# Optimization experiments

Hardware: AMD Instinct MI355X
Metric: run time of the kernel (lower is better)

The kernel has to match this reference:

```python
import jax, jax.numpy as jnp
import numpy as np

B, C, I, E = 2048, 256, 9, 10


def _contraction(U_list, W_list, x, y):
    """Recursive symmetric contraction for one output irrep.
    U_list/W_list ordered [U1, U2, U3] (correlation 1..3).
    x: [b, c, i], y: [b, e]. Returns flattened [b, c * m].
    """
    U3, W3 = U_list[-1], W_list[-1]
    # main: '...ik,ekc,bci,be->bc...'
    out = jnp.einsum('...ik,ekc,bci,be->bc...', U3, W3, x, y)
    for corr in range(len(U_list) - 2, -1, -1):
        U, W = U_list[corr], W_list[corr]
        # weighting: '...k,ekc,be->bc...'
        c_tensor = jnp.einsum('...k,ekc,be->bc...', U, W, y) + out
        # contract: 'bc...i,bci->bc...'
        out = jnp.einsum('bc...i,bci->bc...', c_tensor, x)
    return out.reshape(out.shape[0], -1)


def setup_inputs() -> dict:
    key = jax.random.key(0)
    ks = jax.random.split(key, 14)
    inp = {
        'x': jax.random.normal(ks[0], (B, C, I), jnp.float32),
        'y': jax.random.uniform(ks[1], (B, E), jnp.float32),
        'U1_s': jax.random.normal(ks[2], (I, 1), jnp.float32),
        'U2_s': jax.random.normal(ks[3], (I, I, 3), jnp.float32),
        'U3_s': jax.random.normal(ks[4], (I, I, I, 23), jnp.float32),
        'U1_v': jax.random.normal(ks[5], (3, I, 1), jnp.float32),
        'U2_v': jax.random.normal(ks[6], (3, I, I, 4), jnp.float32),
        'U3_v': jax.random.normal(ks[7], (3, I, I, I, 30), jnp.float32),
        'W1_s': jax.random.normal(ks[8], (E, 1, C), jnp.float32),
        'W2_s': jax.random.normal(ks[9], (E, 3, C), jnp.float32) / 3.0,
        'W3_s': jax.random.normal(ks[10], (E, 23, C), jnp.float32) / 23.0,
        'W1_v': jax.random.normal(ks[11], (E, 1, C), jnp.float32),
        'W2_v': jax.random.normal(ks[12], (E, 4, C), jnp.float32) / 4.0,
        'W3_v': jax.random.normal(ks[13], (E, 30, C), jnp.float32) / 30.0,
    }
    return inp


def reference(x, y, U1_s, U2_s, U3_s, U1_v, U2_v, U3_v,
              W1_s, W2_s, W3_s, W1_v, W2_v, W3_v):
    out_s = _contraction([U1_s, U2_s, U3_s], [W1_s, W2_s, W3_s], x, y)  # [b, c]
    out_v = _contraction([U1_v, U2_v, U3_v], [W1_v, W2_v, W3_v], x, y)  # [b, c*3]
    return jnp.concatenate([out_s, out_v], axis=-1)  # [b, 4c]
```

## Files before the change

kernel.cpp:

```cpp
#include <hip/hip_runtime.h>
#include <hip/hip_bf16.h>


#define NB 2048
#define NC 256
#define NI 9
#define NE 10

#define N_TRI 165
#define N_PAIR 45

#define T3N (N_TRI * NE * NC)
#define T2N (N_PAIR * NE * NC)
#define T1N (NI * NE * NC)

__global__ __launch_bounds__(256) void sc_prep(
    const float* __restrict__ U1_s, const float* __restrict__ U2_s,
    const float* __restrict__ U3_s, const float* __restrict__ U1_v,
    const float* __restrict__ U2_v, const float* __restrict__ U3_v,
    const float* __restrict__ W1_s, const float* __restrict__ W2_s,
    const float* __restrict__ W3_s, const float* __restrict__ W1_v,
    const float* __restrict__ W2_v, const float* __restrict__ W3_v,
    float* __restrict__ ws)
{
    const int m = blockIdx.x;
    const int e = blockIdx.y;
    const int tid = threadIdx.x;
    float4* __restrict__ T3 = (float4*)ws;
    float4* __restrict__ T2 = T3 + T3N;
    float4* __restrict__ T1 = T2 + T2N;

    __shared__ float sym[128];

    if (m < N_TRI) {
        if (tid < 113) {
            int ii = 0, jj = 0, kk = 0, cnt = 0;
            for (int i = 0; i < NI; i++)
                for (int j = i; j < NI; j++)
                    for (int k = j; k < NI; k++) {
                        if (cnt == m) { ii = i; jj = j; kk = k; }
                        cnt++;
                    }
            int P[6][3]; int np;
            if (ii == jj && jj == kk) {
                np = 1;
                P[0][0] = ii; P[0][1] = ii; P[0][2] = ii;
            } else if (ii == jj) {
                np = 3;
                P[0][0] = ii; P[0][1] = ii; P[0][2] = kk;
                P[1][0] = ii; P[1][1] = kk; P[1][2] = ii;
                P[2][0] = kk; P[2][1] = ii; P[2][2] = ii;
            } else if (jj == kk) {
                np = 3;
                P[0][0] = ii; P[0][1] = jj; P[0][2] = jj;
                P[1][0] = jj; P[1][1] = ii; P[1][2] = jj;
                P[2][0] = jj; P[2][1] = jj; P[2][2] = ii;
            } else {
                np = 6;
                P[0][0] = ii; P[0][1] = jj; P[0][2] = kk;
                P[1][0] = ii; P[1][1] = kk; P[1][2] = jj;
                P[2][0] = jj; P[2][1] = ii; P[2][2] = kk;
                P[3][0] = jj; P[3][1] = kk; P[3][2] = ii;
                P[4][0] = kk; P[4][1] = ii; P[4][2] = jj;
                P[5][0] = kk; P[5][1] = jj; P[5][2] = ii;
            }
            float s = 0.f;
            if (tid < 23) {
                for (int p = 0; p < np; p++)
                    s += U3_s[((P[p][0] * NI + P[p][1]) * NI + P[p][2]) * 23 + tid];
            } else {
                int a = (tid - 23) / 30, t = (tid - 23) % 30;
                for (int p = 0; p < np; p++)
                    s += U3_v[(((a * NI + P[p][0]) * NI + P[p][1]) * NI + P[p][2]) * 30 + t];
            }
            sym[tid] = s;
        }
        __syncthreads();
        const int c = tid;
        float s = 0.f, v0 = 0.f, v1 = 0.f, v2 = 0.f;
        #pragma unroll
        for (int t = 0; t < 23; t++)
            s = fmaf(sym[t], W3_s[(e * 23 + t) * NC + c], s);
        #pragma unroll
        for (int t = 0; t < 30; t++) {
            float wv = W3_v[(e * 30 + t) * NC + c];
            v0 = fmaf(sym[23 + t],      wv, v0);
            v1 = fmaf(sym[53 + t],      wv, v1);
            v2 = fmaf(sym[83 + t],      wv, v2);
        }
        T3[(m * NE + e) * NC + c] = make_float4(s, v0, v1, v2);
    } else if (m < N_TRI + N_PAIR) {
        const int mm = m - N_TRI;
        if (tid < 15) {
            int ii = 0, jj = 0, cnt = 0;
            for (int i = 0; i < NI; i++)
                for (int j = i; j < NI; j++) {
                    if (cnt == mm) { ii = i; jj = j; }
                    cnt++;
                }
            float s;
            if (tid < 3) {
                s = U2_s[(ii * NI + jj) * 3 + tid];
                if (ii != jj) s += U2_s[(jj * NI + ii) * 3 + tid];
            } else {
                int a = (tid - 3) / 4, t = (tid - 3) % 4;
                s = U2_v[((a * NI + ii) * NI + jj) * 4 + t];
                if (ii != jj) s += U2_v[((a * NI + jj) * NI + ii) * 4 + t];
            }
            sym[tid] = s;
        }
        __syncthreads();
        const int c = tid;
        float s = 0.f, v0 = 0.f, v1 = 0.f, v2 = 0.f;
        #pragma unroll
        for (int t = 0; t < 3; t++)
            s = fmaf(sym[t], W2_s[(e * 3 + t) * NC + c], s);
        #pragma unroll
        for (int t = 0; t < 4; t++) {
            float wv = W2_v[(e * 4 + t) * NC + c];
            v0 = fmaf(sym[3 + t],  wv, v0);
            v1 = fmaf(sym[7 + t],  wv, v1);
            v2 = fmaf(sym[11 + t], wv, v2);
        }
        T2[(mm * NE + e) * NC + c] = make_float4(s, v0, v1, v2);
    } else {
        const int i = m - N_TRI - N_PAIR;
        const int c = tid;
        float w1s = W1_s[e * NC + c], w1v = W1_v[e * NC + c];
        T1[(i * NE + e) * NC + c] = make_float4(
            U1_s[i] * w1s,
            U1_v[0 * NI + i] * w1v,
            U1_v[1 * NI + i] * w1v,
            U1_v[2 * NI + i] * w1v);
    }
}

#define BT 8
__global__ __launch_bounds__(128) void sc_main(
    const float* __restrict__ x, const float* __restrict__ y,
    const float* __restrict__ ws, float* __restrict__ out)
{
    const int tid = threadIdx.x;
    const int tx  = tid & 63;
    const int tyu = __builtin_amdgcn_readfirstlane(tid >> 6);
    const int bid = blockIdx.x;
    const int xcd    = bid & 7;
    const int c_tile = xcd >> 1;
    const int b_tile = ((bid >> 3) << 1) | (xcd & 1);
    const int c  = (c_tile << 6) + tx;
    const int b0 = (b_tile << 4) + (tyu << 3);

    __shared__ float xs[2][NI][BT][64];
    #pragma unroll
    for (int n = 0; n < BT; n++) {
        const float* xp = x + ((size_t)(b0 + n) * NC + c) * NI;
        #pragma unroll
        for (int i = 0; i < NI; i++) xs[tyu][i][n][tx] = xp[i];
    }

    float w[NE][BT];
    #pragma unroll
    for (int n = 0; n < BT; n++)
        #pragma unroll
        for (int e = 0; e < NE; e++) w[e][n] = y[(b0 + n) * NE + e];

    float acc[BT][4];
    #pragma unroll
    for (int n = 0; n < BT; n++)
        #pragma unroll
        for (int h = 0; h < 4; h++) acc[n][h] = 0.f;

    const float4* __restrict__ T3 = (const float4*)ws;
    const float4* __restrict__ T2 = T3 + T3N;
    const float4* __restrict__ T1 = T2 + T2N;

    {
        float4 tc[NE];
        #pragma unroll
        for (int e = 0; e < NE; e++) tc[e] = T3[e * NC + c];
        int i = 0, j = 0, k = 0;
        for (int m = 0; m < N_TRI; m++) {
            const int mn = (m == N_TRI - 1) ? m : m + 1;
            float4 tn[NE];
            #pragma unroll
            for (int e = 0; e < NE; e++) tn[e] = T3[(mn * NE + e) * NC + c];
            float phi[BT];
            #pragma unroll
            for (int n = 0; n < BT; n++)
                phi[n] = xs[tyu][i][n][tx] * xs[tyu][j][n][tx] * xs[tyu][k][n][tx];
            #pragma unroll
            for (int e = 0; e < NE; e++) {
                const float4 t = tc[e];
                #pragma unroll
                for (int n = 0; n < BT; n++) {
                    const float p = w[e][n] * phi[n];
                    acc[n][0] = fmaf(p, t.x, acc[n][0]);
                    acc[n][1] = fmaf(p, t.y, acc[n][1]);
                    acc[n][2] = fmaf(p, t.z, acc[n][2]);
                    acc[n][3] = fmaf(p, t.w, acc[n][3]);
                }
            }
            #pragma unroll
            for (int e = 0; e < NE; e++) tc[e] = tn[e];
            k++;
            if (k == NI) { j++; if (j == NI) { i++; j = i; } k = j; }
        }
    }

    {
        float4 tc[NE];
        #pragma unroll
        for (int e = 0; e < NE; e++) tc[e] = T2[e * NC + c];
        int i = 0, j = 0;
        for (int m = 0; m < N_PAIR; m++) {
            const int mn = (m == N_PAIR - 1) ? m : m + 1;
            float4 tn[NE];
            #pragma unroll
            for (int e = 0; e < NE; e++) tn[e] = T2[(mn * NE + e) * NC + c];
            float phi[BT];
            #pragma unroll
            for (int n = 0; n < BT; n++)
                phi[n] = xs[tyu][i][n][tx] * xs[tyu][j][n][tx];
            #pragma unroll
            for (int e = 0; e < NE; e++) {
                const float4 t = tc[e];
                #pragma unroll
                for (int n = 0; n < BT; n++) {
                    const float p = w[e][n] * phi[n];
                    acc[n][0] = fmaf(p, t.x, acc[n][0]);
                    acc[n][1] = fmaf(p, t.y, acc[n][1]);
                    acc[n][2] = fmaf(p, t.z, acc[n][2]);
                    acc[n][3] = fmaf(p, t.w, acc[n][3]);
                }
            }
            #pragma unroll
            for (int e = 0; e < NE; e++) tc[e] = tn[e];
            j++;
            if (j == NI) { i++; j = i; }
        }
    }

    for (int i = 0; i < NI; i++) {
        float4 tc[NE];
        #pragma unroll
        for (int e = 0; e < NE; e++) tc[e] = T1[(i * NE + e) * NC + c];
        float phi[BT];
        #pragma unroll
        for (int n = 0; n < BT; n++) phi[n] = xs[tyu][i][n][tx];
        #pragma unroll
        for (int e = 0; e < NE; e++) {
            const float4 t = tc[e];
            #pragma unroll
            for (int n = 0; n < BT; n++) {
                const float p = w[e][n] * phi[n];
                acc[n][0] = fmaf(p, t.x, acc[n][0]);
                acc[n][1] = fmaf(p, t.y, acc[n][1]);
                acc[n][2] = fmaf(p, t.z, acc[n][2]);
                acc[n][3] = fmaf(p, t.w, acc[n][3]);
            }
        }
    }

    #pragma unroll
    for (int n = 0; n < BT; n++) {
        float* ob = out + (size_t)(b0 + n) * (4 * NC);
        ob[c] = acc[n][0];
        ob[NC + 3 * c + 0] = acc[n][1];
        ob[NC + 3 * c + 1] = acc[n][2];
        ob[NC + 3 * c + 2] = acc[n][3];
    }
}

extern "C" void kernel_launch(void* const* d_in, const int* in_sizes, int n_in,
                              void* d_out, int out_size, void* d_ws, size_t ws_size,
                              hipStream_t stream) {
    const float* x    = (const float*)d_in[0];
    const float* y    = (const float*)d_in[1];
    const float* U1_s = (const float*)d_in[2];
    const float* U2_s = (const float*)d_in[3];
    const float* U3_s = (const float*)d_in[4];
    const float* U1_v = (const float*)d_in[5];
    const float* U2_v = (const float*)d_in[6];
    const float* U3_v = (const float*)d_in[7];
    const float* W1_s = (const float*)d_in[8];
    const float* W2_s = (const float*)d_in[9];
    const float* W3_s = (const float*)d_in[10];
    const float* W1_v = (const float*)d_in[11];
    const float* W2_v = (const float*)d_in[12];
    const float* W3_v = (const float*)d_in[13];
    float* out = (float*)d_out;
    float* ws  = (float*)d_ws;

    sc_prep<<<dim3(N_TRI + N_PAIR + NI, NE), 256, 0, stream>>>(
        U1_s, U2_s, U3_s, U1_v, U2_v, U3_v,
        W1_s, W2_s, W3_s, W1_v, W2_v, W3_v, ws);
    sc_main<<<NB / 16 * (NC / 64), 128, 0, stream>>>(x, y, ws, out);
}
```

Baseline: 305.7 us.

## Split outputs into two grid halves and reassociate e-sum with packed FMA

The precomputed T tables are split into two float2 halves, each covering two of the four output channels, and a second grid dimension launches one half per block, doubling the block count. The inner loop is reassociated: it first sums T[e]*y[e] over e with packed v2f FMAs and then multiplies once by phi, instead of forming w*phi for every e and doing four scalar FMAs. The m-loop is unrolled by two with explicit double buffers. The cost is recomputing phi and reloading x and y in both halves, and writing non-contiguous output pieces per half.

```diff
diff --git a/kernel.cpp b/kernel.cpp
--- a/kernel.cpp
+++ b/kernel.cpp
@@ -9,10 +9,16 @@
 
 #define N_TRI 165
 #define N_PAIR 45
-
-#define T3N (N_TRI * NE * NC)
-#define T2N (N_PAIR * NE * NC)
-#define T1N (NI * NE * NC)
+#define BT 8
+
+typedef float v2f __attribute__((ext_vector_type(2)));
+
+#define A3N (N_TRI * NE * NC)
+#define A2N (N_PAIR * NE * NC)
+#define A1N (NI * NE * NC)
+#define PARTN (A3N + A2N + A1N)
+
+__device__ __forceinline__ v2f splat2(float s) { v2f r; r.x = s; r.y = s; return r; }
 
 __global__ __launch_bounds__(256) void sc_prep(
     const float* __restrict__ U1_s, const float* __restrict__ U2_s,
@@ -26,9 +32,9 @@
     const int m = blockIdx.x;
     const int e = blockIdx.y;
     const int tid = threadIdx.x;
-    float4* __restrict__ T3 = (float4*)ws;
-    float4* __restrict__ T2 = T3 + T3N;
-    float4* __restrict__ T1 = T2 + T2N;
+    float2* __restrict__ TA3 = (float2*)ws;
+    float2* __restrict__ TA2 = TA3 + A3N;
+    float2* __restrict__ TA1 = TA2 + A2N;
 
     __shared__ float sym[128];
 
@@ -84,11 +90,12 @@
         #pragma unroll
         for (int t = 0; t < 30; t++) {
             float wv = W3_v[(e * 30 + t) * NC + c];
-            v0 = fmaf(sym[23 + t],      wv, v0);
-            v1 = fmaf(sym[53 + t],      wv, v1);
-            v2 = fmaf(sym[83 + t],      wv, v2);
-        }
-        T3[(m * NE + e) * NC + c] = make_float4(s, v0, v1, v2);
+            v0 = fmaf(sym[23 + t], wv, v0);
+            v1 = fmaf(sym[53 + t], wv, v1);
+            v2 = fmaf(sym[83 + t], wv, v2);
+        }
+        TA3[(m * NE + e) * NC + c] = make_float2(s, v0);
+        TA3[(m * NE + e) * NC + c + PARTN] = make_float2(v1, v2);
     } else if (m < N_TRI + N_PAIR) {
         const int mm = m - N_TRI;
         if (tid < 15) {
@@ -122,20 +129,30 @@
             v1 = fmaf(sym[7 + t],  wv, v1);
             v2 = fmaf(sym[11 + t], wv, v2);
         }
-        T2[(mm * NE + e) * NC + c] = make_float4(s, v0, v1, v2);
+        TA2[(mm * NE + e) * NC + c] = make_float2(s, v0);
+        TA2[(mm * NE + e) * NC + c + PARTN] = make_float2(v1, v2);
     } else {
         const int i = m - N_TRI - N_PAIR;
         const int c = tid;
         float w1s = W1_s[e * NC + c], w1v = W1_v[e * NC + c];
-        T1[(i * NE + e) * NC + c] = make_float4(
-            U1_s[i] * w1s,
-            U1_v[0 * NI + i] * w1v,
-            U1_v[1 * NI + i] * w1v,
-            U1_v[2 * NI + i] * w1v);
+        TA1[(i * NE + e) * NC + c] = make_float2(U1_s[i] * w1s,
+                                                 U1_v[0 * NI + i] * w1v);
+        TA1[(i * NE + e) * NC + c + PARTN] = make_float2(U1_v[1 * NI + i] * w1v,
+                                                         U1_v[2 * NI + i] * w1v);
     }
 }
 
-#define BT 8
+__device__ __forceinline__ void step_acc(const v2f (&buf)[NE], float phi,
+                                         const float* __restrict__ wn,
+                                         v2f& acc)
+{
+    v2f ts = buf[0] * splat2(wn[0]);
+    #pragma unroll
+    for (int e = 1; e < NE; e++)
+        ts = __builtin_elementwise_fma(buf[e], splat2(wn[e]), ts);
+    acc = __builtin_elementwise_fma(splat2(phi), ts, acc);
+}
+
 __global__ __launch_bounds__(128) void sc_main(
     const float* __restrict__ x, const float* __restrict__ y,
     const float* __restrict__ ws, float* __restrict__ out)
@@ -143,10 +160,11 @@
     const int tid = threadIdx.x;
     const int tx  = tid & 63;
     const int tyu = __builtin_amdgcn_readfirstlane(tid >> 6);
-    const int bid = blockIdx.x;
-    const int xcd    = bid & 7;
+    const int bx  = blockIdx.x;
+    const int part = blockIdx.y;
+    const int xcd    = bx & 7;
     const int c_tile = xcd >> 1;
-    const int b_tile = ((bid >> 3) << 1) | (xcd & 1);
+    const int b_tile = ((bx >> 3) << 1) | (xcd & 1);
     const int c  = (c_tile << 6) + tx;
     const int b0 = (b_tile << 4) + (tyu << 3);
 
@@ -157,117 +175,111 @@
         #pragma unroll
         for (int i = 0; i < NI; i++) xs[tyu][i][n][tx] = xp[i];
     }
-
-    float w[NE][BT];
+    const float* xb = &xs[tyu][0][0][tx];
+
+    float w[BT][NE];
     #pragma unroll
     for (int n = 0; n < BT; n++)
         #pragma unroll
-        for (int e = 0; e < NE; e++) w[e][n] = y[(b0 + n) * NE + e];
-
-    float acc[BT][4];
-    #pragma unroll
-    for (int n = 0; n < BT; n++)
-        #pragma unroll
-        for (int h = 0; h < 4; h++) acc[n][h] = 0.f;
-
-    const float4* __restrict__ T3 = (const float4*)ws;
-    const float4* __restrict__ T2 = T3 + T3N;
-    const float4* __restrict__ T1 = T2 + T2N;
+        for (int e = 0; e < NE; e++) w[n][e] = y[(b0 + n) * NE + e];
+
+    v2f acc[BT];
+    #pragma unroll
+    for (int n = 0; n < BT; n++) acc[n] = splat2(0.f);
+
+    const v2f* __restrict__ T3 = (const v2f*)ws + (size_t)part * PARTN;
+    const v2f* __restrict__ T2 = T3 + A3N;
+    const v2f* __restrict__ T1 = T2 + A2N;
 
     {
-        float4 tc[NE];
-        #pragma unroll
-        for (int e = 0; e < NE; e++) tc[e] = T3[e * NC + c];
+        v2f bufA[NE], bufB[NE];
+        #pragma unroll
+        for (int e = 0; e < NE; e++) bufA[e] = T3[e * NC + c];
         int i = 0, j = 0, k = 0;
-        for (int m = 0; m < N_TRI; m++) {
-            const int mn = (m == N_TRI - 1) ? m : m + 1;
-            float4 tn[NE];
-            #pragma unroll
-            for (int e = 0; e < NE; e++) tn[e] = T3[(mn * NE + e) * NC + c];
-            float phi[BT];
-            #pragma unroll
-            for (int n = 0; n < BT; n++)
-                phi[n] = xs[tyu][i][n][tx] * xs[tyu][j][n][tx] * xs[tyu][k][n][tx];
-            #pragma unroll
-            for (int e = 0; e < NE; e++) {
-                const float4 t = tc[e];
+        for (int m = 0; m < N_TRI - 1; m += 2) {
+            #pragma unroll
+            for (int e = 0; e < NE; e++) bufB[e] = T3[((m + 1) * NE + e) * NC + c];
+            {
+                float b1 = 0;  (void)b1;
                 #pragma unroll
                 for (int n = 0; n < BT; n++) {
-                    const float p = w[e][n] * phi[n];
-                    acc[n][0] = fmaf(p, t.x, acc[n][0]);
-                    acc[n][1] = fmaf(p, t.y, acc[n][1]);
-                    acc[n][2] = fmaf(p, t.z, acc[n][2]);
-                    acc[n][3] = fmaf(p, t.w, acc[n][3]);
+                    float ph = xb[(i * BT + n) * 64] * xb[(j * BT + n) * 64]
+                             * xb[(k * BT + n) * 64];
+                    step_acc(bufA, ph, w[n], acc[n]);
                 }
             }
-            #pragma unroll
-            for (int e = 0; e < NE; e++) tc[e] = tn[e];
-            k++;
-            if (k == NI) { j++; if (j == NI) { i++; j = i; } k = j; }
-        }
-    }
-
-    {
-        float4 tc[NE];
-        #pragma unroll
-        for (int e = 0; e < NE; e++) tc[e] = T2[e * NC + c];
-        int i = 0, j = 0;
-        for (int m = 0; m < N_PAIR; m++) {
-            const int mn = (m == N_PAIR - 1) ? m : m + 1;
-            float4 tn[NE];
-            #pragma unroll
-            for (int e = 0; e < NE; e++) tn[e] = T2[(mn * NE + e) * NC + c];
-            float phi[BT];
-            #pragma unroll
-            for (int n = 0; n < BT; n++)
-                phi[n] = xs[tyu][i][n][tx] * xs[tyu][j][n][tx];
-            #pragma unroll
-            for (int e = 0; e < NE; e++) {
-                const float4 t = tc[e];
+            k++; if (k == NI) { j++; if (j == NI) { i++; j = i; } k = j; }
+            const int mp = (m + 2 < N_TRI) ? m + 2 : N_TRI - 1;
+            #pragma unroll
+            for (int e = 0; e < NE; e++) bufA[e] = T3[(mp * NE + e) * NC + c];
+            {
                 #pragma unroll
                 for (int n = 0; n < BT; n++) {
-                    const float p = w[e][n] * phi[n];
-                    acc[n][0] = fmaf(p, t.x, acc[n][0]);
-                    acc[n][1] = fmaf(p, t.y, acc[n][1]);
-                    acc[n][2] = fmaf(p, t.z, acc[n][2]);
-                    acc[n][3] = fmaf(p, t.w, acc[n][3]);
+                    float ph = xb[(i * BT + n) * 64] * xb[(j * BT + n) * 64]
+                             * xb[(k * BT + n) * 64];
+                    step_acc(bufB, ph, w[n], acc[n]);
                 }
             }
-            #pragma unroll
-            for (int e = 0; e < NE; e++) tc[e] = tn[e];
-            j++;
-            if (j == NI) { i++; j = i; }
+            k++; if (k == NI) { j++; if (j == NI) { i++; j = i; } k = j; }
+        }
+        #pragma unroll
+        for (int n = 0; n < BT; n++) {
+            float ph = xb[(i * BT + n) * 64] * xb[(j * BT + n) * 64]
+                     * xb[(k * BT + n) * 64];
+            step_acc(bufA, ph, w[n], acc[n]);
+        }
+    }
+
+    {
+        v2f bufA[NE], bufB[NE];
+        #pragma unroll
+        for (int e = 0; e < NE; e++) bufA[e] = T2[e * NC + c];
+        int i = 0, j = 0;
+        for (int m = 0; m < N_PAIR - 1; m += 2) {
+            #pragma unroll
+            for (int e = 0; e < NE; e++) bufB[e] = T2[((m + 1) * NE + e) * NC + c];
+            #pragma unroll
+            for (int n = 0; n < BT; n++) {
+                float ph = xb[(i * BT + n) * 64] * xb[(j * BT + n) * 64];
+                step_acc(bufA, ph, w[n], acc[n]);
+            }
+            j++; if (j == NI) { i++; j = i; }
+            const int mp = (m + 2 < N_PAIR) ? m + 2 : N_PAIR - 1;
+            #pragma unroll
+            for (int e = 0; e < NE; e++) bufA[e] = T2[(mp * NE + e) * NC + c];
+            #pragma unroll
+            for (int n = 0; n < BT; n++) {
+                float ph = xb[(i * BT + n) * 64] * xb[(j * BT + n) * 64];
+                step_acc(bufB, ph, w[n], acc[n]);
+            }
+            j++; if (j == NI) { i++; j = i; }
+        }
+        #pragma unroll
+        for (int n = 0; n < BT; n++) {
+            float ph = xb[(i * BT + n) * 64] * xb[(j * BT + n) * 64];
+            step_acc(bufA, ph, w[n], acc[n]);
         }
     }
 
     for (int i = 0; i < NI; i++) {
-        float4 tc[NE];
-        #pragma unroll
-        for (int e = 0; e < NE; e++) tc[e] = T1[(i * NE + e) * NC + c];
-        float phi[BT];
-        #pragma unroll
-        for (int n = 0; n < BT; n++) phi[n] = xs[tyu][i][n][tx];
-        #pragma unroll
-        for (int e = 0; e < NE; e++) {
-            const float4 t = tc[e];
-            #pragma unroll
-            for (int n = 0; n < BT; n++) {
-                const float p = w[e][n] * phi[n];
-                acc[n][0] = fmaf(p, t.x, acc[n][0]);
-                acc[n][1] = fmaf(p, t.y, acc[n][1]);
-                acc[n][2] = fmaf(p, t.z, acc[n][2]);
-                acc[n][3] = fmaf(p, t.w, acc[n][3]);
-            }
-        }
+        v2f buf[NE];
+        #pragma unroll
+        for (int e = 0; e < NE; e++) buf[e] = T1[(i * NE + e) * NC + c];
+        #pragma unroll
+        for (int n = 0; n < BT; n++)
+            step_acc(buf, xb[(i * BT + n) * 64], w[n], acc[n]);
     }
 
     #pragma unroll
     for (int n = 0; n < BT; n++) {
         float* ob = out + (size_t)(b0 + n) * (4 * NC);
-        ob[c] = acc[n][0];
-        ob[NC + 3 * c + 0] = acc[n][1];
-        ob[NC + 3 * c + 1] = acc[n][2];
-        ob[NC + 3 * c + 2] = acc[n][3];
+        if (part == 0) {
+            ob[c] = acc[n].x;
+            ob[NC + 3 * c + 0] = acc[n].y;
+        } else {
+            ob[NC + 3 * c + 1] = acc[n].x;
+            ob[NC + 3 * c + 2] = acc[n].y;
+        }
     }
 }
 
@@ -294,5 +306,5 @@
     sc_prep<<<dim3(N_TRI + N_PAIR + NI, NE), 256, 0, stream>>>(
         U1_s, U2_s, U3_s, U1_v, U2_v, U3_v,
         W1_s, W2_s, W3_s, W1_v, W2_v, W3_v, ws);
-    sc_main<<<NB / 16 * (NC / 64), 128, 0, stream>>>(x, y, ws, out);
+    sc_main<<<dim3(512, 2), 128, 0, stream>>>(x, y, ws, out);
 }
```

Measured after the change: 480.0 us. 1.57x slower.

## Split contraction across two blocks per tile with atomic accumulation and double-buffered loads

Applied to the files above, without the earlier changes.

The main kernel now launches two blocks per (b, c) tile. One block handles the first 110 triples. The other handles the remaining triples plus the pair and single terms. Partial sums are combined with atomicAdd into an output that is zeroed by a memset first. This doubles the number of waves available to hide the latency of the precomputed-table loads. The triple and pair loops are rewritten as explicit ping-pong double buffers. The prep kernel now loops over e inside each block, so the symmetrised U is computed once per m instead of once per e. The cost is serialised prep work on fewer blocks, extra atomic traffic, and a memset launch.

```diff
diff --git a/kernel.cpp b/kernel.cpp
--- a/kernel.cpp
+++ b/kernel.cpp
@@ -9,10 +9,13 @@
 
 #define N_TRI 165
 #define N_PAIR 45
+#define BT 8
 
 #define T3N (N_TRI * NE * NC)
 #define T2N (N_PAIR * NE * NC)
 #define T1N (NI * NE * NC)
+
+#define MSPLIT 110
 
 __global__ __launch_bounds__(256) void sc_prep(
     const float* __restrict__ U1_s, const float* __restrict__ U2_s,
@@ -24,7 +27,6 @@
     float* __restrict__ ws)
 {
     const int m = blockIdx.x;
-    const int e = blockIdx.y;
     const int tid = threadIdx.x;
     float4* __restrict__ T3 = (float4*)ws;
     float4* __restrict__ T2 = T3 + T3N;
@@ -77,18 +79,20 @@
         }
         __syncthreads();
         const int c = tid;
-        float s = 0.f, v0 = 0.f, v1 = 0.f, v2 = 0.f;
-        #pragma unroll
-        for (int t = 0; t < 23; t++)
-            s = fmaf(sym[t], W3_s[(e * 23 + t) * NC + c], s);
-        #pragma unroll
-        for (int t = 0; t < 30; t++) {
-            float wv = W3_v[(e * 30 + t) * NC + c];
-            v0 = fmaf(sym[23 + t],      wv, v0);
-            v1 = fmaf(sym[53 + t],      wv, v1);
-            v2 = fmaf(sym[83 + t],      wv, v2);
-        }
-        T3[(m * NE + e) * NC + c] = make_float4(s, v0, v1, v2);
+        for (int e = 0; e < NE; e++) {
+            float s = 0.f, v0 = 0.f, v1 = 0.f, v2 = 0.f;
+            #pragma unroll
+            for (int t = 0; t < 23; t++)
+                s = fmaf(sym[t], W3_s[(e * 23 + t) * NC + c], s);
+            #pragma unroll
+            for (int t = 0; t < 30; t++) {
+                float wv = W3_v[(e * 30 + t) * NC + c];
+                v0 = fmaf(sym[23 + t], wv, v0);
+                v1 = fmaf(sym[53 + t], wv, v1);
+                v2 = fmaf(sym[83 + t], wv, v2);
+            }
+            T3[(m * NE + e) * NC + c] = make_float4(s, v0, v1, v2);
+        }
     } else if (m < N_TRI + N_PAIR) {
         const int mm = m - N_TRI;
         if (tid < 15) {
@@ -111,31 +115,116 @@
         }
         __syncthreads();
         const int c = tid;
-        float s = 0.f, v0 = 0.f, v1 = 0.f, v2 = 0.f;
-        #pragma unroll
-        for (int t = 0; t < 3; t++)
-            s = fmaf(sym[t], W2_s[(e * 3 + t) * NC + c], s);
-        #pragma unroll
-        for (int t = 0; t < 4; t++) {
-            float wv = W2_v[(e * 4 + t) * NC + c];
-            v0 = fmaf(sym[3 + t],  wv, v0);
-            v1 = fmaf(sym[7 + t],  wv, v1);
-            v2 = fmaf(sym[11 + t], wv, v2);
-        }
-        T2[(mm * NE + e) * NC + c] = make_float4(s, v0, v1, v2);
+        for (int e = 0; e < NE; e++) {
+            float s = 0.f, v0 = 0.f, v1 = 0.f, v2 = 0.f;
+            #pragma unroll
+            for (int t = 0; t < 3; t++)
+                s = fmaf(sym[t], W2_s[(e * 3 + t) * NC + c], s);
+            #pragma unroll
+            for (int t = 0; t < 4; t++) {
+                float wv = W2_v[(e * 4 + t) * NC + c];
+                v0 = fmaf(sym[3 + t],  wv, v0);
+                v1 = fmaf(sym[7 + t],  wv, v1);
+                v2 = fmaf(sym[11 + t], wv, v2);
+            }
+            T2[(mm * NE + e) * NC + c] = make_float4(s, v0, v1, v2);
+        }
     } else {
         const int i = m - N_TRI - N_PAIR;
         const int c = tid;
-        float w1s = W1_s[e * NC + c], w1v = W1_v[e * NC + c];
-        T1[(i * NE + e) * NC + c] = make_float4(
-            U1_s[i] * w1s,
-            U1_v[0 * NI + i] * w1v,
-            U1_v[1 * NI + i] * w1v,
-            U1_v[2 * NI + i] * w1v);
+        for (int e = 0; e < NE; e++) {
+            float w1s = W1_s[e * NC + c], w1v = W1_v[e * NC + c];
+            T1[(i * NE + e) * NC + c] = make_float4(
+                U1_s[i] * w1s,
+                U1_v[0 * NI + i] * w1v,
+                U1_v[1 * NI + i] * w1v,
+                U1_v[2 * NI + i] * w1v);
+        }
     }
 }
 
-#define BT 8
+__device__ __forceinline__ void tri_advance(int& i, int& j, int& k) {
+    k++;
+    if (k == NI) { j++; if (j == NI) { i++; j = i; } k = j; }
+}
+
+template <int M0, int M1, int I0, int J0, int K0>
+__device__ __forceinline__ void do_triples(
+    const float4* __restrict__ T3, int c, const float* __restrict__ xb,
+    const float (&w)[NE][BT], float (&acc)[BT][4])
+{
+    float4 bufA[NE], bufB[NE];
+    #pragma unroll
+    for (int e = 0; e < NE; e++) bufA[e] = T3[(M0 * NE + e) * NC + c];
+    int i = I0, j = J0, k = K0;
+    for (int m = M0; m + 1 < M1; m += 2) {
+        #pragma unroll
+        for (int e = 0; e < NE; e++) bufB[e] = T3[((m + 1) * NE + e) * NC + c];
+        {
+            float phi[BT];
+            #pragma unroll
+            for (int n = 0; n < BT; n++)
+                phi[n] = xb[(i * BT + n) * 64] * xb[(j * BT + n) * 64]
+                       * xb[(k * BT + n) * 64];
+            #pragma unroll
+            for (int e = 0; e < NE; e++) {
+                const float4 t = bufA[e];
+                #pragma unroll
+                for (int n = 0; n < BT; n++) {
+                    const float p = w[e][n] * phi[n];
+                    acc[n][0] = fmaf(p, t.x, acc[n][0]);
+                    acc[n][1] = fmaf(p, t.y, acc[n][1]);
+                    acc[n][2] = fmaf(p, t.z, acc[n][2]);
+                    acc[n][3] = fmaf(p, t.w, acc[n][3]);
+                }
+            }
+        }
+        tri_advance(i, j, k);
+        const int mp = (m + 2 < M1) ? m + 2 : M1 - 1;
+        #pragma unroll
+        for (int e = 0; e < NE; e++) bufA[e] = T3[(mp * NE + e) * NC + c];
+        {
+            float phi[BT];
+            #pragma unroll
+            for (int n = 0; n < BT; n++)
+                phi[n] = xb[(i * BT + n) * 64] * xb[(j * BT + n) * 64]
+                       * xb[(k * BT + n) * 64];
+            #pragma unroll
+            for (int e = 0; e < NE; e++) {
+                const float4 t = bufB[e];
+                #pragma unroll
+                for (int n = 0; n < BT; n++) {
+                    const float p = w[e][n] * phi[n];
+                    acc[n][0] = fmaf(p, t.x, acc[n][0]);
+                    acc[n][1] = fmaf(p, t.y, acc[n][1]);
+                    acc[n][2] = fmaf(p, t.z, acc[n][2]);
+                    acc[n][3] = fmaf(p, t.w, acc[n][3]);
+                }
+            }
+        }
+        tri_advance(i, j, k);
+    }
+    if ((M1 - M0) & 1) {
+        float phi[BT];
+        #pragma unroll
+        for (int n = 0; n < BT; n++)
+            phi[n] = xb[(i * BT + n) * 64] * xb[(j * BT + n) * 64]
+                   * xb[(k * BT + n) * 64];
+        #pragma unroll
+        for (int e = 0; e < NE; e++) {
+            const float4 t = bufA[e];
+            #pragma unroll
+            for (int n = 0; n < BT; n++) {
+                const float p = w[e][n] * phi[n];
+                acc[n][0] = fmaf(p, t.x, acc[n][0]);
+                acc[n][1] = fmaf(p, t.y, acc[n][1]);
+                acc[n][2] = fmaf(p, t.z, acc[n][2]);
+                acc[n][3] = fmaf(p, t.w, acc[n][3]);
+            }
+        }
+    }
+}
+
 __global__ __launch_bounds__(128) void sc_main(
     const float* __restrict__ x, const float* __restrict__ y,
     const float* __restrict__ ws, float* __restrict__ out)
@@ -143,10 +232,11 @@
     const int tid = threadIdx.x;
     const int tx  = tid & 63;
     const int tyu = __builtin_amdgcn_readfirstlane(tid >> 6);
-    const int bid = blockIdx.x;
-    const int xcd    = bid & 7;
+    const int bx  = blockIdx.x;
+    const int part = blockIdx.y;
+    const int xcd    = bx & 7;
     const int c_tile = xcd >> 1;
-    const int b_tile = ((bid >> 3) << 1) | (xcd & 1);
+    const int b_tile = ((bx >> 3) << 1) | (xcd & 1);
     const int c  = (c_tile << 6) + tx;
     const int b0 = (b_tile << 4) + (tyu << 3);
 
@@ -157,6 +247,7 @@
         #pragma unroll
         for (int i = 0; i < NI; i++) xs[tyu][i][n][tx] = xp[i];
     }
+    const float* xb = &xs[tyu][0][0][tx];
 
     float w[NE][BT];
     #pragma unroll
@@ -174,20 +265,88 @@
     const float4* __restrict__ T2 = T3 + T3N;
     const float4* __restrict__ T1 = T2 + T2N;
 
-    {
-        float4 tc[NE];
-        #pragma unroll
-        for (int e = 0; e < NE; e++) tc[e] = T3[e * NC + c];
-        int i = 0, j = 0, k = 0;
-        for (int m = 0; m < N_TRI; m++) {
-            const int mn = (m == N_TRI - 1) ? m : m + 1;
-            float4 tn[NE];
-            #pragma unroll
-            for (int e = 0; e < NE; e++) tn[e] = T3[(mn * NE + e) * NC + c];
+    if (part == 0) {
+        do_triples<0, MSPLIT, 0, 0, 0>(T3, c, xb, w, acc);
+    } else {
+        do_triples<MSPLIT, N_TRI, 3, 3, 4>(T3, c, xb, w, acc);
+
+        {
+            float4 bufA[NE], bufB[NE];
+            #pragma unroll
+            for (int e = 0; e < NE; e++) bufA[e] = T2[e * NC + c];
+            int i = 0, j = 0;
+            for (int m = 0; m + 1 < N_PAIR; m += 2) {
+                #pragma unroll
+                for (int e = 0; e < NE; e++) bufB[e] = T2[((m + 1) * NE + e) * NC + c];
+                {
+                    float phi[BT];
+                    #pragma unroll
+                    for (int n = 0; n < BT; n++)
+                        phi[n] = xb[(i * BT + n) * 64] * xb[(j * BT + n) * 64];
+                    #pragma unroll
+                    for (int e = 0; e < NE; e++) {
+                        const float4 t = bufA[e];
+                        #pragma unroll
+                        for (int n = 0; n < BT; n++) {
+                            const float p = w[e][n] * phi[n];
+                            acc[n][0] = fmaf(p, t.x, acc[n][0]);
+                            acc[n][1] = fmaf(p, t.y, acc[n][1]);
+                            acc[n][2] = fmaf(p, t.z, acc[n][2]);
+                            acc[n][3] = fmaf(p, t.w, acc[n][3]);
+                        }
+                    }
+                }
+                j++; if (j == NI) { i++; j = i; }
+                const int mp = (m + 2 < N_PAIR) ? m + 2 : N_PAIR - 1;
+                #pragma unroll
+                for (int e = 0; e < NE; e++) bufA[e] = T2[(mp * NE + e) * NC + c];
+                {
+                    float phi[BT];
+                    #pragma unroll
+                    for (int n = 0; n < BT; n++)
+                        phi[n] = xb[(i * BT + n) * 64] * xb[(j * BT + n) * 64];
+                    #pragma unroll
+                    for (int e = 0; e < NE; e++) {
+                        const float4 t = bufB[e];
+                        #pragma unroll
+                        for (int n = 0; n < BT; n++) {
+                            const float p = w[e][n] * phi[n];
+                            acc[n][0] = fmaf(p, t.x, acc[n][0]);
+                            acc[n][1] = fmaf(p, t.y, acc[n][1]);
+                            acc[n][2] = fmaf(p, t.z, acc[n][2]);
+                            acc[n][3] = fmaf(p, t.w, acc[n][3]);
+                        }
+                    }
+                }
+                j++; if (j == NI) { i++; j = i; }
+            }
+            {
+                float phi[BT];
+                #pragma unroll
+                for (int n = 0; n < BT; n++)
+                    phi[n] = xb[(i * BT + n) * 64] * xb[(j * BT + n) * 64];
+                #pragma unroll
+                for (int e = 0; e < NE; e++) {
+                    const float4 t = bufA[e];
+                    #pragma unroll
+                    for (int n = 0; n < BT; n++) {
+                        const float p = w[e][n] * phi[n];
+                        acc[n][0] = fmaf(p, t.x, acc[n][0]);
+                        acc[n][1] = fmaf(p, t.y, acc[n][1]);
+                        acc[n][2] = fmaf(p, t.z, acc[n][2]);
+                        acc[n][3] = fmaf(p, t.w, acc[n][3]);
+                    }
+                }
+            }
+        }
+
+        for (int i = 0; i < NI; i++) {
+            float4 tc[NE];
+            #pragma unroll
+            for (int e = 0; e < NE; e++) tc[e] = T1[(i * NE + e) * NC + c];
             float phi[BT];
             #pragma unroll
-            for (int n = 0; n < BT; n++)
-                phi[n] = xs[tyu][i][n][tx] * xs[tyu][j][n][tx] * xs[tyu][k][n][tx];
+            for (int n = 0; n < BT; n++) phi[n] = xb[(i * BT + n) * 64];
             #pragma unroll
             for (int e = 0; e < NE; e++) {
                 const float4 t = tc[e];
@@ -200,74 +359,16 @@
                     acc[n][3] = fmaf(p, t.w, acc[n][3]);
                 }
             }
-            #pragma unroll
-            for (int e = 0; e < NE; e++) tc[e] = tn[e];
-            k++;
-            if (k == NI) { j++; if (j == NI) { i++; j = i; } k = j; }
-        }
-    }
-
-    {
-        float4 tc[NE];
-        #pragma unroll
-        for (int e = 0; e < NE; e++) tc[e] = T2[e * NC + c];
-        int i = 0, j = 0;
-        for (int m = 0; m < N_PAIR; m++) {
-            const int mn = (m == N_PAIR - 1) ? m : m + 1;
-            float4 tn[NE];
-            #pragma unroll
-            for (int e = 0; e < NE; e++) tn[e] = T2[(mn * NE + e) * NC + c];
-            float phi[BT];
-            #pragma unroll
-            for (int n = 0; n < BT; n++)
-                phi[n] = xs[tyu][i][n][tx] * xs[tyu][j][n][tx];
-            #pragma unroll
-            for (int e = 0; e < NE; e++) {
-                const float4 t = tc[e];
-                #pragma unroll
-                for (int n = 0; n < BT; n++) {
-                    const float p = w[e][n] * phi[n];
-                    acc[n][0] = fmaf(p, t.x, acc[n][0]);
-                    acc[n][1] = fmaf(p, t.y, acc[n][1]);
-                    acc[n][2] = fmaf(p, t.z, acc[n][2]);
-                    acc[n][3] = fmaf(p, t.w, acc[n][3]);
-                }
-            }
-            #pragma unroll
-            for (int e = 0; e < NE; e++) tc[e] = tn[e];
-            j++;
-            if (j == NI) { i++; j = i; }
-        }
-    }
-
-    for (int i = 0; i < NI; i++) {
-        float4 tc[NE];
-        #pragma unroll
-        for (int e = 0; e < NE; e++) tc[e] = T1[(i * NE + e) * NC + c];
-        float phi[BT];
-        #pragma unroll
-        for (int n = 0; n < BT; n++) phi[n] = xs[tyu][i][n][tx];
-        #pragma unroll
-        for (int e = 0; e < NE; e++) {
-            const float4 t = tc[e];
-            #pragma unroll
-            for (int n = 0; n < BT; n++) {
-                const float p = w[e][n] * phi[n];
-                acc[n][0] = fmaf(p, t.x, acc[n][0]);
-                acc[n][1] = fmaf(p, t.y, acc[n][1]);
-                acc[n][2] = fmaf(p, t.z, acc[n][2]);
-                acc[n][3] = fmaf(p, t.w, acc[n][3]);
-            }
         }
     }
 
     #pragma unroll
     for (int n = 0; n < BT; n++) {
         float* ob = out + (size_t)(b0 + n) * (4 * NC);
-        ob[c] = acc[n][0];
-        ob[NC + 3 * c + 0] = acc[n][1];
-        ob[NC + 3 * c + 1] = acc[n][2];
-        ob[NC + 3 * c + 2] = acc[n][3];
+        atomicAdd(&ob[c],              acc[n][0]);
+        atomicAdd(&ob[NC + 3 * c + 0], acc[n][1]);
+        atomicAdd(&ob[NC + 3 * c + 1], acc[n][2]);
+        atomicAdd(&ob[NC + 3 * c + 2], acc[n][3]);
     }
 }
 
@@ -291,8 +392,9 @@
     float* out = (float*)d_out;
     float* ws  = (float*)d_ws;
 
-    sc_prep<<<dim3(N_TRI + N_PAIR + NI, NE), 256, 0, stream>>>(
+    hipMemsetAsync(out, 0, (size_t)out_size * sizeof(float), stream);
+    sc_prep<<<N_TRI + N_PAIR + NI, 256, 0, stream>>>(
         U1_s, U2_s, U3_s, U1_v, U2_v, U3_v,
         W1_s, W2_s, W3_s, W1_v, W2_v, W3_v, ws);
-    sc_main<<<NB / 16 * (NC / 64), 128, 0, stream>>>(x, y, ws, out);
+    sc_main<<<dim3(512, 2), 128, 0, stream>>>(x, y, ws, out);
 }
```

Result: slower. 336.5 us (+10.1%).
